# Kernel tuning notes

Hardware: AMD Instinct MI355X
Metric: run time of the kernel (lower is better)

The kernel has to match this reference:

```python
import jax, jax.numpy as jnp
import numpy as np

B, T, D, M = 8, 4096, 64, 1024  # batch, frames, embedding_dim, codebook size


def setup_inputs() -> dict:
    key = jax.random.key(0)
    k1, k2, k3 = jax.random.split(key, 3)
    x = jax.random.normal(k1, (B, D, T), dtype=jnp.float32)          # (B, channels=D, T)
    embedding = jax.random.normal(k2, (M, D), dtype=jnp.float32)     # codebook
    # Precomputed Gumbel noise, matching torch: -log(-log(clamp(U, eps, 1-eps)))
    eps = jnp.finfo(jnp.float32).eps
    u = jax.random.uniform(k3, (B * T, M), dtype=jnp.float32)
    gumbels = -jnp.log(-jnp.log(jnp.clip(u, eps, 1.0 - eps)))
    log_var_q = jnp.float32(0.0)
    temperature = jnp.float32(0.5)
    return {"x": x, "embedding": embedding, "log_var_q": log_var_q,
            "gumbels": gumbels, "temperature": temperature}


def reference(x, embedding, log_var_q, gumbels, temperature):
    B_, D_, T_ = x.shape
    M_ = embedding.shape[0]
    xt = jnp.swapaxes(x, 1, 2)                 # (B, T, D)
    x_flat = xt.reshape(-1, D_)                # (N, D)
    precision = jnp.exp(-log_var_q)            # scalar
    # 0.5 * precision * ||x - e||^2, via the GEMM expansion (fused cdist)
    sq = (jnp.sum(x_flat * x_flat, axis=1, keepdims=True)
          + jnp.sum(embedding * embedding, axis=1)[None, :]
          - 2.0 * x_flat @ embedding.T)        # (N, M)
    distances = 0.5 * precision * sq
    indices = jnp.argmin(distances, axis=-1)   # (N,)
    logits = -distances
    # gumbel-softmax (soft)
    encodings = jax.nn.softmax((logits + gumbels) / temperature, axis=-1)  # (N, M)
    quantized = (encodings @ embedding).reshape(B_, T_, D_)                # (B, T, D)
    logits3 = logits.reshape(B_, T_, M_)
    log_probs = jax.nn.log_softmax(logits3, axis=-1)
    probs = jnp.exp(log_probs)
    recon = 0.5 * precision * jnp.sum((xt - quantized) ** 2, axis=(1, 2))  # (B,)
    neg_entropy = jnp.sum(probs * log_probs, axis=(1, 2))                  # (B,)
    loss = jnp.mean(recon + neg_entropy)
    # perplexity over hard assignments
    one_hot = jax.nn.one_hot(indices, M_, dtype=jnp.float32)               # (N, M)
    avg_probs = jnp.mean(one_hot, axis=0)
    perplexity = jnp.exp(-jnp.sum(avg_probs * jnp.log(avg_probs + 1e-10)))
    return jnp.swapaxes(quantized, 1, 2), loss, perplexity
```

## Files before the change

kernel.cpp:

```cpp
#include <hip/hip_runtime.h>

#define T_DIM 4096
#define D_DIM 64
#define M_DIM 1024
#define N_ROWS 32768
#define TR 16
#define NT 512
#define NW 8

typedef __attribute__((ext_vector_type(8))) short bf16x8;
typedef __attribute__((ext_vector_type(4))) float f32x4;

#define WS_BF16_OFF 4096

__device__ __forceinline__ short f2bfs(float f) {
  union { float f; unsigned u; } v; v.f = f;
  unsigned r = v.u + 0x7fffu + ((v.u >> 16) & 1u);
  return (short)(r >> 16);
}
__device__ __forceinline__ float bf2f(short h) {
  union { unsigned u; float f; } v; v.u = ((unsigned)(unsigned short)h) << 16;
  return v.f;
}
__device__ __forceinline__ void cvt8(const float* p, bf16x8& h8, bf16x8& l8) {
  float4 a = *(const float4*)p, b = *(const float4*)(p + 4);
  float v[8] = {a.x, a.y, a.z, a.w, b.x, b.y, b.z, b.w};
#pragma unroll
  for (int i = 0; i < 8; ++i) {
    short h = f2bfs(v[i]);
    h8[i] = h;
    l8[i] = f2bfs(v[i] - bf2f(h));
  }
}

__global__ void vq_conv(const float* __restrict__ emb, float* __restrict__ ws) {
  __shared__ short s_h[64][72], s_l[64][72];
  const int tid = threadIdx.x;
  const int mb = blockIdx.x * 64;
  short* EH = (short*)(ws + WS_BF16_OFF);
  short* EL = EH + 65536;
  short* ETH = EL + 65536;
  short* ETL = ETH + 65536;
#pragma unroll
  for (int i = 0; i < 16; ++i) {
    int lin = tid + 256 * i;
    int ml = lin >> 6, d = lin & 63;
    float v = emb[(size_t)(mb + ml) * 64 + d];
    short h = f2bfs(v);
    short l = f2bfs(v - bf2f(h));
    EH[(size_t)(mb + ml) * 64 + d] = h;
    EL[(size_t)(mb + ml) * 64 + d] = l;
    s_h[d][ml] = h;
    s_l[d][ml] = l;
  }
  if (tid < 64) {
    const float* e = emb + (size_t)(mb + tid) * 64;
    float s = 0.f;
#pragma unroll
    for (int d = 0; d < 64; d += 4) {
      float4 v = *(const float4*)(e + d);
      s += v.x * v.x + v.y * v.y + v.z * v.z + v.w * v.w;
    }
    ws[mb + tid] = s;
    ws[M_DIM + mb + tid] = 0.f;
  }
  if (blockIdx.x == 0 && tid == 0) ws[2 * M_DIM] = 0.f;
  __syncthreads();
#pragma unroll
  for (int i = 0; i < 16; ++i) {
    int lin = tid + 256 * i;
    int d = lin >> 6, ml = lin & 63;
    ETH[(size_t)d * 1024 + mb + ml] = s_h[d][ml];
    ETL[(size_t)d * 1024 + mb + ml] = s_l[d][ml];
  }
}

__global__ __launch_bounds__(NT, 4) void vq_main(
    const float* __restrict__ x, const float* __restrict__ emb,
    const float* __restrict__ lvq, const float* __restrict__ gum,
    const float* __restrict__ temp, float* __restrict__ outq,
    float* __restrict__ ws) {
  __shared__ float s_x[TR][68];
  __shared__ float s_xx[TR];
  __shared__ float s_qp[NW][TR][68];
  __shared__ float2 s_stA[NW][TR];
  __shared__ float4 s_stB[NW][TR];
  __shared__ float s_red[NW];

  const int tid = threadIdx.x;
  const int lane = tid & 63;
  const int wl = tid >> 6;
  const int mq = lane >> 4;
  const int mn = lane & 15;
  const int n0 = blockIdx.x * TR;
  const int b = n0 >> 12;
  const int t0 = n0 & (T_DIM - 1);
  const float precision = __expf(-lvq[0]);
  const float inv_temp = 1.0f / temp[0];
  const float* eew = ws;
  float* counts = ws + M_DIM;
  float* accum = ws + 2 * M_DIM;
  const short* EH = (const short*)(ws + WS_BF16_OFF);
  const short* EL = EH + 65536;
  const short* ETH = EL + 65536;
  const short* ETL = ETH + 65536;

  {
    int tt = tid & 15, d0 = tid >> 4;
    s_x[tt][d0] = x[((size_t)b << 18) + ((size_t)d0 << 12) + (size_t)(t0 + tt)];
    s_x[tt][d0 + 32] =
        x[((size_t)b << 18) + ((size_t)(d0 + 32) << 12) + (size_t)(t0 + tt)];
  }
  __syncthreads();
  if (tid < TR) {
    float s = 0.f;
#pragma unroll
    for (int d = 0; d < D_DIM; ++d) { float v = s_x[tid][d]; s += v * v; }
    s_xx[tid] = s;
  }
  __syncthreads();

  float gpre[8][4];
  {
    const float* gp0 = gum + ((size_t)(n0 + mq * 4) << 10) + (size_t)(wl * 128 + mn);
#pragma unroll
    for (int reg = 0; reg < 4; ++reg) {
#pragma unroll
      for (int tt = 0; tt < 8; ++tt)
        gpre[tt][reg] = gp0[((size_t)reg << 10) + tt * 16];
    }
  }
  __builtin_amdgcn_sched_barrier(0);

  f32x4 acc[8];
  {
    bf16x8 ah0, al0, ah1, al1;
    cvt8(&s_x[mn][mq * 8], ah0, al0);
    cvt8(&s_x[mn][32 + mq * 8], ah1, al1);
#pragma unroll
    for (int tt = 0; tt < 8; ++tt) acc[tt] = (f32x4){0.f, 0.f, 0.f, 0.f};
#pragma unroll
    for (int tt = 0; tt < 8; ++tt) {
      int m0 = wl * 128 + tt * 16;
      const short* bp = EH + (m0 + mn) * 64 + mq * 8;
      const short* lp = EL + (m0 + mn) * 64 + mq * 8;
      bf16x8 bh0 = *(const bf16x8*)bp;
      bf16x8 bh1 = *(const bf16x8*)(bp + 32);
      bf16x8 bl0 = *(const bf16x8*)lp;
      bf16x8 bl1 = *(const bf16x8*)(lp + 32);
      acc[tt] = __builtin_amdgcn_mfma_f32_16x16x32_bf16(ah0, bh0, acc[tt], 0, 0, 0);
      acc[tt] = __builtin_amdgcn_mfma_f32_16x16x32_bf16(ah1, bh1, acc[tt], 0, 0, 0);
      acc[tt] = __builtin_amdgcn_mfma_f32_16x16x32_bf16(al0, bh0, acc[tt], 0, 0, 0);
      acc[tt] = __builtin_amdgcn_mfma_f32_16x16x32_bf16(al1, bh1, acc[tt], 0, 0, 0);
      acc[tt] = __builtin_amdgcn_mfma_f32_16x16x32_bf16(ah0, bl0, acc[tt], 0, 0, 0);
      acc[tt] = __builtin_amdgcn_mfma_f32_16x16x32_bf16(ah1, bl1, acc[tt], 0, 0, 0);
    }
    float xx4[4];
#pragma unroll
    for (int reg = 0; reg < 4; ++reg) xx4[reg] = s_xx[mq * 4 + reg];
#pragma unroll
    for (int tt = 0; tt < 8; ++tt) {
      float eev = eew[wl * 128 + tt * 16 + mn];
#pragma unroll
      for (int reg = 0; reg < 4; ++reg)
        acc[tt][reg] = precision * (acc[tt][reg] - 0.5f * (xx4[reg] + eev));
    }
  }

  float Mx[4]; int Mi[4];
#pragma unroll
  for (int reg = 0; reg < 4; ++reg) {
    float mx = acc[0][reg]; int mi = wl * 128 + mn;
#pragma unroll
    for (int tt = 1; tt < 8; ++tt) {
      float v = acc[tt][reg];
      int m = wl * 128 + tt * 16 + mn;
      if (v > mx) { mx = v; mi = m; }
    }
#pragma unroll
    for (int off = 1; off <= 8; off <<= 1) {
      float omx = __shfl_xor(mx, off);
      int omi = __shfl_xor(mi, off);
      if (omx > mx || (omx == mx && omi < mi)) { mx = omx; mi = omi; }
    }
    if (mn == 0) s_stA[wl][mq * 4 + reg] = make_float2(mx, __int_as_float(mi));
  }
  __syncthreads();
#pragma unroll
  for (int reg = 0; reg < 4; ++reg) {
    int token = mq * 4 + reg;
    float2 a0 = s_stA[0][token];
    float mx = a0.x; int mi = __float_as_int(a0.y);
#pragma unroll
    for (int w = 1; w < NW; ++w) {
      float2 aw = s_stA[w][token];
      int i2 = __float_as_int(aw.y);
      if (aw.x > mx || (aw.x == mx && i2 < mi)) { mx = aw.x; mi = i2; }
    }
    Mx[reg] = mx; Mi[reg] = mi;
  }
  float partial = 0.f;
  if (wl == 0 && mn == 0) {
#pragma unroll
    for (int reg = 0; reg < 4; ++reg) atomicAdd(counts + Mi[reg], 1.0f);
  }

  float Zs[4] = {0.f, 0.f, 0.f, 0.f}, As[4] = {0.f, 0.f, 0.f, 0.f}, Gm[4];
#pragma unroll
  for (int reg = 0; reg < 4; ++reg) {
    float gm = -1e30f;
#pragma unroll
    for (int tt = 0; tt < 8; ++tt) {
      float g = gpre[tt][reg];
      float s = acc[tt][reg];
      float a = s - Mx[reg];
      float e = __expf(a);
      Zs[reg] += e; As[reg] += a * e;
      float gv = (s + g) * inv_temp;
      acc[tt][reg] = gv;
      gm = fmaxf(gm, gv);
    }
    Gm[reg] = gm;
  }
#pragma unroll
  for (int reg = 0; reg < 4; ++reg) {
#pragma unroll
    for (int off = 1; off <= 8; off <<= 1) {
      Zs[reg] += __shfl_xor(Zs[reg], off);
      As[reg] += __shfl_xor(As[reg], off);
      Gm[reg] = fmaxf(Gm[reg], __shfl_xor(Gm[reg], off));
    }
  }
  float Zg[4] = {0.f, 0.f, 0.f, 0.f};
#pragma unroll
  for (int tt = 0; tt < 8; ++tt) {
#pragma unroll
    for (int reg = 0; reg < 4; ++reg) {
      float p = __expf(acc[tt][reg] - Gm[reg]);
      acc[tt][reg] = p;
      Zg[reg] += p;
    }
  }
#pragma unroll
  for (int reg = 0; reg < 4; ++reg) {
#pragma unroll
    for (int off = 1; off <= 8; off <<= 1) Zg[reg] += __shfl_xor(Zg[reg], off);
    if (mn == 0)
      s_stB[wl][mq * 4 + reg] = make_float4(Zs[reg], As[reg], Gm[reg], Zg[reg]);
  }
  __syncthreads();
  float invZg[4];
#pragma unroll
  for (int reg = 0; reg < 4; ++reg) {
    int token = mq * 4 + reg;
    float gmax = -1e30f;
#pragma unroll
    for (int w = 0; w < NW; ++w) gmax = fmaxf(gmax, s_stB[w][token].z);
    float zs = 0.f, as = 0.f, zg = 0.f;
#pragma unroll
    for (int w = 0; w < NW; ++w) {
      float4 v = s_stB[w][token];
      zs += v.x; as += v.y;
      zg += v.w * __expf(v.z - gmax);
    }
    invZg[reg] = __expf(Gm[reg] - gmax) / zg;
    if (wl == 0 && mn == 0) partial += as / zs - __logf(zs);
  }

  {
    f32x4 q[4];
#pragma unroll
    for (int nt = 0; nt < 4; ++nt) q[nt] = (f32x4){0.f, 0.f, 0.f, 0.f};
    float* sp = &s_qp[wl][0][0];
#pragma unroll
    for (int ks = 0; ks < 4; ++ks) {
#pragma unroll
      for (int reg = 0; reg < 4; ++reg) {
        sp[(mq * 4 + reg) * 36 + mn]      = acc[2 * ks][reg] * invZg[reg];
        sp[(mq * 4 + reg) * 36 + 16 + mn] = acc[2 * ks + 1][reg] * invZg[reg];
      }
      bf16x8 ph, pl;
      cvt8(&sp[mn * 36 + mq * 8], ph, pl);
      int k0 = wl * 128 + ks * 32;
#pragma unroll
      for (int nt = 0; nt < 4; ++nt) {
        const short* bp = ETH + (nt * 16 + mn) * 1024 + k0 + mq * 8;
        const short* lp = ETL + (nt * 16 + mn) * 1024 + k0 + mq * 8;
        bf16x8 bh = *(const bf16x8*)bp;
        bf16x8 bl = *(const bf16x8*)lp;
        q[nt] = __builtin_amdgcn_mfma_f32_16x16x32_bf16(ph, bh, q[nt], 0, 0, 0);
        q[nt] = __builtin_amdgcn_mfma_f32_16x16x32_bf16(pl, bh, q[nt], 0, 0, 0);
        q[nt] = __builtin_amdgcn_mfma_f32_16x16x32_bf16(ph, bl, q[nt], 0, 0, 0);
      }
    }
#pragma unroll
    for (int nt = 0; nt < 4; ++nt)
#pragma unroll
      for (int reg = 0; reg < 4; ++reg)
        s_qp[wl][mq * 4 + reg][nt * 16 + mn] = q[nt][reg];
  }
  __syncthreads();

  {
    int r = tid & 15, dq = tid >> 4;
    int d = dq * 2;
    float2 qs = {0.f, 0.f};
#pragma unroll
    for (int w = 0; w < NW; ++w) {
      float2 v = *(const float2*)&s_qp[w][r][d];
      qs.x += v.x; qs.y += v.y;
    }
    int t = t0 + r;
    float* ob = outq + ((size_t)b << 18) + (size_t)t;
    ob[(size_t)(d + 0) << 12] = qs.x;
    ob[(size_t)(d + 1) << 12] = qs.y;
    float2 xv = *(const float2*)&s_x[r][d];
    float dx0 = xv.x - qs.x, dx1 = xv.y - qs.y;
    partial += 0.5f * precision * (dx0 * dx0 + dx1 * dx1);
  }
#pragma unroll
  for (int off = 32; off; off >>= 1) partial += __shfl_xor(partial, off);
  if (lane == 0) s_red[wl] = partial;
  __syncthreads();
  if (tid == 0) {
    float s = 0.f;
#pragma unroll
    for (int w = 0; w < NW; ++w) s += s_red[w];
    atomicAdd(accum, s);
  }
}

__global__ void vq_finalize(const float* __restrict__ ws, float* __restrict__ out) {
  __shared__ float red[4];
  int tid = threadIdx.x;
  float h = 0.f;
  for (int m = tid; m < M_DIM; m += 256) {
    float avg = ws[M_DIM + m] * (1.0f / 32768.0f);
    h += avg * __logf(avg + 1e-10f);
  }
#pragma unroll
  for (int off = 32; off; off >>= 1) h += __shfl_xor(h, off);
  int lane = tid & 63, wave = tid >> 6;
  if (lane == 0) red[wave] = h;
  __syncthreads();
  if (tid == 0) {
    out[0] = ws[2 * M_DIM] * 0.125f;
    out[1] = __expf(-(red[0] + red[1] + red[2] + red[3]));
  }
}

extern "C" void kernel_launch(void* const* d_in, const int* in_sizes, int n_in,
                              void* d_out, int out_size, void* d_ws, size_t ws_size,
                              hipStream_t stream) {
  const float* x = (const float*)d_in[0];
  const float* emb = (const float*)d_in[1];
  const float* lvq = (const float*)d_in[2];
  const float* gum = (const float*)d_in[3];
  const float* temp = (const float*)d_in[4];
  float* out = (float*)d_out;
  float* ws = (float*)d_ws;

  hipLaunchKernelGGL(vq_conv, dim3(16), dim3(256), 0, stream, emb, ws);
  hipLaunchKernelGGL(vq_main, dim3(N_ROWS / TR), dim3(NT), 0, stream,
                     x, emb, lvq, gum, temp, out, ws);
  hipLaunchKernelGGL(vq_finalize, dim3(1), dim3(256), 0, stream, ws,
                     out + (size_t)2097152);
}
```

Baseline: 325.1 us.

## Drop per-row norm term and merge argmax into a single online-softmax reduction

Removes the ||x||^2 computation and its barrier, since a per-row constant does not change argmin or the softmaxes. The cross-wave max is now merged together with the softmax partial sums using local maxima and rescaling, which removes one shared-memory barrier stage. The Gumbel loads move after the MFMA loop, presumably to cut register pressure or change latency hiding. The trade-off is some extra exp work in the merge, and the Gumbel load latency is no longer overlapped with the GEMM.

```diff
diff --git a/kernel.cpp b/kernel.cpp
--- a/kernel.cpp
+++ b/kernel.cpp
@@ -81,10 +81,9 @@
     const float* __restrict__ temp, float* __restrict__ outq,
     float* __restrict__ ws) {
   __shared__ float s_x[TR][68];
-  __shared__ float s_xx[TR];
   __shared__ float s_qp[NW][TR][68];
-  __shared__ float2 s_stA[NW][TR];
-  __shared__ float4 s_stB[NW][TR];
+  __shared__ float4 s_st1[NW][TR];
+  __shared__ float2 s_st2[NW][TR];
   __shared__ float s_red[NW];
 
   const int tid = threadIdx.x;
@@ -96,6 +95,7 @@
   const int b = n0 >> 12;
   const int t0 = n0 & (T_DIM - 1);
   const float precision = __expf(-lvq[0]);
+  const float halfprec = 0.5f * precision;
   const float inv_temp = 1.0f / temp[0];
   const float* eew = ws;
   float* counts = ws + M_DIM;
@@ -112,25 +112,6 @@
         x[((size_t)b << 18) + ((size_t)(d0 + 32) << 12) + (size_t)(t0 + tt)];
   }
   __syncthreads();
-  if (tid < TR) {
-    float s = 0.f;
-#pragma unroll
-    for (int d = 0; d < D_DIM; ++d) { float v = s_x[tid][d]; s += v * v; }
-    s_xx[tid] = s;
-  }
-  __syncthreads();
-
-  float gpre[8][4];
-  {
-    const float* gp0 = gum + ((size_t)(n0 + mq * 4) << 10) + (size_t)(wl * 128 + mn);
-#pragma unroll
-    for (int reg = 0; reg < 4; ++reg) {
-#pragma unroll
-      for (int tt = 0; tt < 8; ++tt)
-        gpre[tt][reg] = gp0[((size_t)reg << 10) + tt * 16];
-    }
-  }
-  __builtin_amdgcn_sched_barrier(0);
 
   f32x4 acc[8];
   {
@@ -155,54 +136,44 @@
       acc[tt] = __builtin_amdgcn_mfma_f32_16x16x32_bf16(ah0, bl0, acc[tt], 0, 0, 0);
       acc[tt] = __builtin_amdgcn_mfma_f32_16x16x32_bf16(ah1, bl1, acc[tt], 0, 0, 0);
     }
-    float xx4[4];
-#pragma unroll
-    for (int reg = 0; reg < 4; ++reg) xx4[reg] = s_xx[mq * 4 + reg];
-#pragma unroll
-    for (int tt = 0; tt < 8; ++tt) {
-      float eev = eew[wl * 128 + tt * 16 + mn];
-#pragma unroll
-      for (int reg = 0; reg < 4; ++reg)
-        acc[tt][reg] = precision * (acc[tt][reg] - 0.5f * (xx4[reg] + eev));
-    }
-  }
-
-  float Mx[4]; int Mi[4];
-#pragma unroll
-  for (int reg = 0; reg < 4; ++reg) {
-    float mx = acc[0][reg]; int mi = wl * 128 + mn;
+  }
+
+  float gpre[8][4];
+  {
+    const float* gp0 = gum + ((size_t)(n0 + mq * 4) << 10) + (size_t)(wl * 128 + mn);
+#pragma unroll
+    for (int reg = 0; reg < 4; ++reg) {
+#pragma unroll
+      for (int tt = 0; tt < 8; ++tt)
+        gpre[tt][reg] = gp0[((size_t)reg << 10) + tt * 16];
+    }
+  }
+
+#pragma unroll
+  for (int tt = 0; tt < 8; ++tt) {
+    float eev = eew[wl * 128 + tt * 16 + mn];
+#pragma unroll
+    for (int reg = 0; reg < 4; ++reg)
+      acc[tt][reg] = precision * acc[tt][reg] - halfprec * eev;
+  }
+
+  float ml[4]; int mi[4];
+#pragma unroll
+  for (int reg = 0; reg < 4; ++reg) {
+    float mx = acc[0][reg]; int ix = wl * 128 + mn;
 #pragma unroll
     for (int tt = 1; tt < 8; ++tt) {
       float v = acc[tt][reg];
       int m = wl * 128 + tt * 16 + mn;
-      if (v > mx) { mx = v; mi = m; }
+      if (v > mx) { mx = v; ix = m; }
     }
 #pragma unroll
     for (int off = 1; off <= 8; off <<= 1) {
       float omx = __shfl_xor(mx, off);
-      int omi = __shfl_xor(mi, off);
-      if (omx > mx || (omx == mx && omi < mi)) { mx = omx; mi = omi; }
-    }
-    if (mn == 0) s_stA[wl][mq * 4 + reg] = make_float2(mx, __int_as_float(mi));
-  }
-  __syncthreads();
-#pragma unroll
-  for (int reg = 0; reg < 4; ++reg) {
-    int token = mq * 4 + reg;
-    float2 a0 = s_stA[0][token];
-    float mx = a0.x; int mi = __float_as_int(a0.y);
-#pragma unroll
-    for (int w = 1; w < NW; ++w) {
-      float2 aw = s_stA[w][token];
-      int i2 = __float_as_int(aw.y);
-      if (aw.x > mx || (aw.x == mx && i2 < mi)) { mx = aw.x; mi = i2; }
-    }
-    Mx[reg] = mx; Mi[reg] = mi;
-  }
-  float partial = 0.f;
-  if (wl == 0 && mn == 0) {
-#pragma unroll
-    for (int reg = 0; reg < 4; ++reg) atomicAdd(counts + Mi[reg], 1.0f);
+      int oix = __shfl_xor(ix, off);
+      if (omx > mx || (omx == mx && oix < ix)) { mx = omx; ix = oix; }
+    }
+    ml[reg] = mx; mi[reg] = ix;
   }
 
   float Zs[4] = {0.f, 0.f, 0.f, 0.f}, As[4] = {0.f, 0.f, 0.f, 0.f}, Gm[4];
@@ -213,7 +184,7 @@
     for (int tt = 0; tt < 8; ++tt) {
       float g = gpre[tt][reg];
       float s = acc[tt][reg];
-      float a = s - Mx[reg];
+      float a = s - ml[reg];
       float e = __expf(a);
       Zs[reg] += e; As[reg] += a * e;
       float gv = (s + g) * inv_temp;
@@ -245,26 +216,49 @@
   for (int reg = 0; reg < 4; ++reg) {
 #pragma unroll
     for (int off = 1; off <= 8; off <<= 1) Zg[reg] += __shfl_xor(Zg[reg], off);
-    if (mn == 0)
-      s_stB[wl][mq * 4 + reg] = make_float4(Zs[reg], As[reg], Gm[reg], Zg[reg]);
-  }
-  __syncthreads();
+    if (mn == 0) {
+      s_st1[wl][mq * 4 + reg] =
+          make_float4(ml[reg], __int_as_float(mi[reg]), Zs[reg], As[reg]);
+      s_st2[wl][mq * 4 + reg] = make_float2(Gm[reg], Zg[reg]);
+    }
+  }
+  __syncthreads();
+
   float invZg[4];
+  float partial = 0.f;
 #pragma unroll
   for (int reg = 0; reg < 4; ++reg) {
     int token = mq * 4 + reg;
-    float gmax = -1e30f;
-#pragma unroll
-    for (int w = 0; w < NW; ++w) gmax = fmaxf(gmax, s_stB[w][token].z);
-    float zs = 0.f, as = 0.f, zg = 0.f;
+    float M = -1e30f; int bi = 0x7fffffff;
 #pragma unroll
     for (int w = 0; w < NW; ++w) {
-      float4 v = s_stB[w][token];
-      zs += v.x; as += v.y;
-      zg += v.w * __expf(v.z - gmax);
-    }
-    invZg[reg] = __expf(Gm[reg] - gmax) / zg;
-    if (wl == 0 && mn == 0) partial += as / zs - __logf(zs);
+      float4 v = s_st1[w][token];
+      int iv = __float_as_int(v.y);
+      if (v.x > M || (v.x == M && iv < bi)) { M = v.x; bi = iv; }
+    }
+    float zs = 0.f, as = 0.f;
+#pragma unroll
+    for (int w = 0; w < NW; ++w) {
+      float4 v = s_st1[w][token];
+      float d = v.x - M;
+      float ed = __expf(d);
+      zs += ed * v.z;
+      as += ed * (v.w + d * v.z);
+    }
+    float GM = -1e30f;
+#pragma unroll
+    for (int w = 0; w < NW; ++w) GM = fmaxf(GM, s_st2[w][token].x);
+    float zg = 0.f;
+#pragma unroll
+    for (int w = 0; w < NW; ++w) {
+      float2 u = s_st2[w][token];
+      zg += u.y * __expf(u.x - GM);
+    }
+    invZg[reg] = __expf(Gm[reg] - GM) / zg;
+    if (wl == 0 && mn == 0) {
+      partial += as / zs - __logf(zs);
+      atomicAdd(counts + bi, 1.0f);
+    }
   }
 
   {
```

Measured after the change: 328.6 us. No clear change (+1.1%).
